# Kernel tuning notes

Hardware: AMD Instinct MI355X
Metric: run time of the kernel (lower is better)

Reference implementation:

```python
import jax, jax.numpy as jnp
import numpy as np

H = 128
OUT = 3
N_C = 50000
N_F = 150000
E_C = 400000
N_MP = 2


def _layernorm(x, g, b, eps=1e-5):
    mu = jnp.mean(x, axis=-1, keepdims=True)
    xc = x - mu
    var = jnp.mean(xc * xc, axis=-1, keepdims=True)
    return xc * jax.lax.rsqrt(var + eps) * g + b


def _seg_mean(v, idx, n):
    s = jax.ops.segment_sum(v, idx, num_segments=n)
    c = jax.ops.segment_sum(jnp.ones((v.shape[0],), v.dtype), idx, num_segments=n)
    return s / jnp.maximum(c, 1.0)[:, None]


def _mp_pass(x, ea, ei, n_nodes, eW0, eb0, eW1, eb1, eg, ebt, nW0, nb0, nW1, nb1, ng, nbt):
    src, dst = ei[0], ei[1]
    for i in range(N_MP):
        # edge update: gather endpoints, concat, 2-layer MLP, residual + LN
        t = jnp.concatenate([x[src], x[dst], ea], axis=1)  # [E, 3H]
        t = jax.nn.elu(t @ eW0[i] + eb0[i])
        t = t @ eW1[i] + eb1[i]
        ea = _layernorm(ea + t, eg[i], ebt[i])
        # scatter-mean aggregate edges to target nodes (EdgeAggregator)
        agg = _seg_mean(ea, dst, n_nodes)  # [N, H]
        xt = jnp.concatenate([x, agg], axis=1)  # [N, 2H]
        xt = jax.nn.elu(xt @ nW0[i] + nb0[i])
        xt = xt @ nW1[i] + nb1[i]
        x = _layernorm(x + xt, ng[i], nbt[i])
    return x, ea


def setup_inputs() -> dict:
    key = jax.random.key(0)
    ks = jax.random.split(key, 40)

    def nrm(k, shape, fan):
        return jax.random.normal(k, shape, jnp.float32) * np.float32(1.0 / np.sqrt(fan))

    inp = {}
    inp["x"] = jax.random.normal(ks[0], (N_C, H), jnp.float32)
    inp["edge_attr"] = jax.random.normal(ks[1], (E_C, H), jnp.float32)
    inp["pos_c"] = jax.random.uniform(ks[2], (N_C, 2), jnp.float32)
    inp["pos_f"] = jax.random.uniform(ks[3], (N_F, 2), jnp.float32)
    inp["edge_index_c"] = jax.random.randint(ks[4], (2, E_C), 0, N_C)
    clusters = jax.random.randint(ks[5], (N_F,), 0, N_C)
    inp["clusters"] = clusters
    # one f2c edge per fine node: row0 = fine idx, row1 = its coarse cluster
    inp["edge_index_f2c"] = jnp.stack([jnp.arange(N_F), clusters])
    # edge_up_mps params (stacked over N_MP layers)
    inp["eW0"] = nrm(ks[6], (N_MP, 3 * H, H), 3 * H)
    inp["eb0"] = jnp.zeros((N_MP, H), jnp.float32)
    inp["eW1"] = nrm(ks[7], (N_MP, H, H), H)
    inp["eb1"] = jnp.zeros((N_MP, H), jnp.float32)
    inp["eg"] = jnp.ones((N_MP, H), jnp.float32)
    inp["ebt"] = jnp.zeros((N_MP, H), jnp.float32)
    # node_up_mps params
    inp["nW0"] = nrm(ks[8], (N_MP, 2 * H, H), 2 * H)
    inp["nb0"] = jnp.zeros((N_MP, H), jnp.float32)
    inp["nW1"] = nrm(ks[9], (N_MP, H, H), H)
    inp["nb1"] = jnp.zeros((N_MP, H), jnp.float32)
    inp["ng"] = jnp.ones((N_MP, H), jnp.float32)
    inp["nbt"] = jnp.zeros((N_MP, H), jnp.float32)
    # edge_decoder_c2f_mlp
    inp["dW0"] = nrm(ks[10], (2, H), 2)
    inp["db0"] = jnp.zeros((H,), jnp.float32)
    inp["dW1"] = nrm(ks[11], (H, H), H)
    inp["db1"] = jnp.zeros((H,), jnp.float32)
    # upsample_mlp + norm
    inp["uW0"] = nrm(ks[12], (2 * H, H), 2 * H)
    inp["ub0"] = jnp.zeros((H,), jnp.float32)
    inp["uW1"] = nrm(ks[13], (H, H), H)
    inp["ub1"] = jnp.zeros((H,), jnp.float32)
    inp["ug"] = jnp.ones((H,), jnp.float32)
    inp["ubt"] = jnp.zeros((H,), jnp.float32)
    # output embedding
    inp["oW"] = nrm(ks[14], (H, OUT), H)
    inp["ob"] = jnp.zeros((OUT,), jnp.float32)
    return inp


def reference(x, edge_attr, pos_c, pos_f, edge_index_c, clusters, edge_index_f2c,
              eW0, eb0, eW1, eb1, eg, ebt, nW0, nb0, nW1, nb1, ng, nbt,
              dW0, db0, dW1, db1, uW0, ub0, uW1, ub1, ug, ubt, oW, ob):
    # coarse-level message passing (m = 0)
    x, ea = _mp_pass(x, edge_attr, edge_index_c, N_C,
                     eW0, eb0, eW1, eb1, eg, ebt, nW0, nb0, nW1, nb1, ng, nbt)
    # upsample coarse -> fine (depth = 2, l_char[0] = 1.0)
    c2f = edge_index_f2c[::-1]  # row0 = coarse idx, row1 = fine idx
    eac = (pos_c[c2f[0]] - pos_f[c2f[1]]) / 1.0  # [N_F, 2]
    eac = jax.nn.elu(eac @ dW0 + db0)
    eac = jax.nn.elu(eac @ dW1 + db1)
    xg = x[clusters]  # [N_F, H]
    t = jnp.concatenate([eac, xg], axis=1)
    t = jax.nn.elu(t @ uW0 + ub0)
    t = jax.nn.elu(t @ uW1 + ub1)
    t = _layernorm(eac + t, ug, ubt)
    x = _seg_mean(t, c2f[1], N_F)  # aggregate c2f edges onto fine nodes
    # fine-level message passing (m stays 0 in the original code -> same weights, same coarse edges)
    x, ea = _mp_pass(x, ea, edge_index_c, N_F,
                     eW0, eb0, eW1, eb1, eg, ebt, nW0, nb0, nW1, nb1, ng, nbt)
    x = jax.nn.elu(x @ oW + ob)
    return (x, edge_index_c)
```

## Files before the change

### kernel.cpp

```cpp
#include <hip/hip_runtime.h>


#define HD   128
#define NC   50000
#define NF   150000
#define ECNT 400000
#define OUTD 3
#define SCB  512
#define NB_SCAN ((NF + SCB - 1) / SCB)

typedef unsigned short u16;
typedef unsigned int   u32;
typedef short bf16x8 __attribute__((ext_vector_type(8)));
typedef float f32x4  __attribute__((ext_vector_type(4)));

__device__ __forceinline__ float bf2f(u32 u){ return __uint_as_float(u << 16); }
__device__ __forceinline__ u32 cvtpk(float a, float b){
  u32 r; asm("v_cvt_pk_bf16_f32 %0, %1, %2" : "=v"(r) : "v"(a), "v"(b)); return r;
}
__device__ __forceinline__ u16 f2bf(float f){ return (u16)cvtpk(f, f); }
__device__ __forceinline__ u32 addpk(u32 a, u32 b){
  return cvtpk(bf2f(a & 0xffffu) + bf2f(b & 0xffffu),
               __uint_as_float(a & 0xffff0000u) + __uint_as_float(b & 0xffff0000u));
}
__device__ __forceinline__ float eluf(float x){ return x > 0.f ? x : __expf(x) - 1.f; }
__device__ __forceinline__ int SW(int row, int byte){ return row * 256 + (byte ^ ((row & 7) << 4)); }


__global__ void prep_all_kernel(const float* __restrict__ eW0, const float* __restrict__ eW1,
                                const float* __restrict__ nW0, const float* __restrict__ nW1,
                                const float* __restrict__ uW0, const float* __restrict__ uW1,
                                const float* __restrict__ dW1,
                                u16* c_eW0, u16* c_eW1, u16* c_nW0, u16* c_nW1,
                                u16* c_uW0, u16* c_uW1, u16* c_dW1)
{
  int b = blockIdx.x;
  const float* src; u16* dst; int kb;
  if      (b <  384){ src = eW0; dst = c_eW0; kb = b * 2; }
  else if (b <  512){ src = eW1; dst = c_eW1; kb = (b - 384) * 2; }
  else if (b <  768){ src = nW0; dst = c_nW0; kb = (b - 512) * 2; }
  else if (b <  896){ src = nW1; dst = c_nW1; kb = (b - 768) * 2; }
  else if (b < 1024){ src = uW0; dst = c_uW0; kb = (b - 896) * 2; }
  else if (b < 1088){ src = uW1; dst = c_uW1; kb = (b - 1024) * 2; }
  else              { src = dW1; dst = c_dW1; kb = (b - 1088) * 2; }
  int t = threadIdx.x;
  int k = kb + (t >> 7), j = t & 127;
  dst[(((k >> 3) * HD + j) << 3) + (k & 7)] = f2bf(src[k * HD + j]);
}

__global__ void f32_to_bf16_vec(const float* __restrict__ in, u16* __restrict__ out, int n8){
  int i = blockIdx.x * blockDim.x + threadIdx.x;
  if (i >= n8) return;
  float4 f0 = ((const float4*)in)[i * 2];
  float4 f1 = ((const float4*)in)[i * 2 + 1];
  ((uint4*)out)[i] = make_uint4(cvtpk(f0.x,f0.y), cvtpk(f0.z,f0.w), cvtpk(f1.x,f1.y), cvtpk(f1.z,f1.w));
}

__global__ void deg_kernel(const int* __restrict__ ei, int* __restrict__ deg){
  int e = blockIdx.x * blockDim.x + threadIdx.x;
  if (e < ECNT) atomicAdd(&deg[ei[ECNT + e]], 1);
}

__global__ void scanA_kernel(const int* __restrict__ deg, int* __restrict__ part){
  __shared__ int s[SCB];
  int t = threadIdx.x, i = blockIdx.x * SCB + t;
  s[t] = (i < NF) ? deg[i] : 0;
  __syncthreads();
  for (int off = SCB/2; off; off >>= 1){ if (t < off) s[t] += s[t + off]; __syncthreads(); }
  if (t == 0) part[blockIdx.x] = s[0];
}

__global__ void scanB_kernel(int* __restrict__ part){
  __shared__ int s[SCB];
  int t = threadIdx.x;
  int v = (t < NB_SCAN) ? part[t] : 0;
  s[t] = v; __syncthreads();
  for (int off = 1; off < SCB; off <<= 1){
    int x = (t >= off) ? s[t - off] : 0;
    __syncthreads(); s[t] += x; __syncthreads();
  }
  if (t < NB_SCAN) part[t] = s[t] - v;
}

__global__ void scanC_kernel(const int* __restrict__ deg, const int* __restrict__ part,
                             int* __restrict__ rowptr){
  __shared__ int s[SCB];
  int t = threadIdx.x, i = blockIdx.x * SCB + t;
  int v = (i < NF) ? deg[i] : 0;
  s[t] = v; __syncthreads();
  for (int off = 1; off < SCB; off <<= 1){
    int x = (t >= off) ? s[t - off] : 0;
    __syncthreads(); s[t] += x; __syncthreads();
  }
  int excl = part[blockIdx.x] + s[t] - v;
  if (i < NF) rowptr[i] = excl;
  if (i == NF - 1) rowptr[NF] = excl + v;
}

__global__ void build_perm_kernel(const int* __restrict__ ei, int* __restrict__ cursor,
                                  int* __restrict__ perm, int* __restrict__ esrc,
                                  int* __restrict__ edst){
  int e = blockIdx.x * blockDim.x + threadIdx.x;
  if (e >= ECNT) return;
  int sI = ei[e], d = ei[ECNT + e];
  int p = atomicAdd(&cursor[d], 1);
  perm[p] = e; esrc[p] = sI; edst[p] = d;
}

__global__ void permute_ea_kernel(const float* __restrict__ ea_in, const int* __restrict__ perm,
                                  u16* __restrict__ ea_s){
  int i = blockIdx.x * blockDim.x + threadIdx.x;
  if (i >= ECNT * 16) return;
  int p = i >> 4, c = i & 15;
  int e = perm[p];
  const float4* src = (const float4*)(ea_in + (size_t)e * HD + c * 8);
  float4 f0 = src[0], f1 = src[1];
  ((uint4*)ea_s)[(size_t)p * 16 + c] =
      make_uint4(cvtpk(f0.x,f0.y), cvtpk(f0.z,f0.w), cvtpk(f1.x,f1.y), cvtpk(f1.z,f1.w));
}

template<int NOUT>
__global__ __launch_bounds__(256, 4)
void lin_kernel(const u16* __restrict__ Wa, const u16* __restrict__ Wb,
                const u16* __restrict__ x, u16* __restrict__ oA, u16* __restrict__ oB,
                int n_rows)
{
  __shared__ __align__(16) char ldsA[32 * 256];
  const int tid = threadIdx.x, lane = tid & 63, wid = tid >> 6;
  const int ln = lane & 15, kq = lane >> 4, ncol = wid * 32;

  const int row0 = blockIdx.x << 5;
  #pragma unroll
  for (int c = 0; c < 2; ++c){
    int i = tid + c * 256, row = i >> 4, kk = i & 15, rg = row0 + row;
    if (rg < n_rows)
      *(uint4*)(ldsA + SW(row, kk * 16)) = *(const uint4*)(x + (((size_t)rg) << 7) + (kk << 3));
  }
  __syncthreads();
  bf16x8 af[4][2];
  #pragma unroll
  for (int k0 = 0; k0 < 4; ++k0){
    af[k0][0] = *(const bf16x8*)(ldsA + SW(ln,      k0 * 64 + (kq << 4)));
    af[k0][1] = *(const bf16x8*)(ldsA + SW(16 + ln, k0 * 64 + (kq << 4)));
  }

  const u16* Ws[2] = {Wa, Wb};
  u16*       Os[2] = {oA, oB};
  const f32x4 zz = {0.f, 0.f, 0.f, 0.f};
  #pragma unroll
  for (int w = 0; w < NOUT; ++w){
    const u16* wp = Ws[w];
    asm volatile("" : "+v"(wp));
    uint4 bfr[4][2];
    #pragma unroll
    for (int k0 = 0; k0 < 4; ++k0)
      #pragma unroll
      for (int nt = 0; nt < 2; ++nt)
        bfr[k0][nt] = *(const uint4*)(wp + (((size_t)((k0*4 + kq)*HD + ncol + nt*16 + ln)) << 3));
    f32x4 cc[2][2] = {{zz, zz}, {zz, zz}};
    #pragma unroll
    for (int k0 = 0; k0 < 4; ++k0){
      bf16x8 w0 = __builtin_bit_cast(bf16x8, bfr[k0][0]);
      bf16x8 w1 = __builtin_bit_cast(bf16x8, bfr[k0][1]);
      cc[0][0] = __builtin_amdgcn_mfma_f32_16x16x32_bf16(af[k0][0], w0, cc[0][0], 0, 0, 0);
      cc[0][1] = __builtin_amdgcn_mfma_f32_16x16x32_bf16(af[k0][0], w1, cc[0][1], 0, 0, 0);
      cc[1][0] = __builtin_amdgcn_mfma_f32_16x16x32_bf16(af[k0][1], w0, cc[1][0], 0, 0, 0);
      cc[1][1] = __builtin_amdgcn_mfma_f32_16x16x32_bf16(af[k0][1], w1, cc[1][1], 0, 0, 0);
    }
    u16* op = Os[w];
    #pragma unroll
    for (int mi = 0; mi < 2; ++mi)
      #pragma unroll
      for (int nt = 0; nt < 2; ++nt)
        #pragma unroll
        for (int r = 0; r < 4; ++r){
          int rg = row0 + mi * 16 + kq * 4 + r;
          if (rg < n_rows) op[(size_t)rg * HD + ncol + nt * 16 + ln] = f2bf(cc[mi][nt][r]);
        }
  }
}

enum { M_EDGE = 0, M_NODE = 1, M_DEC12 = 2 };

template<int MODE>
__global__ __launch_bounds__(256, 4)
void mlp_kernel(const u16* __restrict__ W0c, const u16* __restrict__ W1c,
                const u16* __restrict__ W2c,
                const float* __restrict__ b0, const float* __restrict__ b1,
                const float* __restrict__ b2,
                const float* __restrict__ gw, const float* __restrict__ bw,
                const u16* __restrict__ tabA, const u16* __restrict__ addP,
                const u16* __restrict__ addQ, const u16* __restrict__ resid,
                const int* __restrict__ esrc, const int* __restrict__ edst,
                const int* __restrict__ rowptr, const u16* __restrict__ eatab,
                const int* __restrict__ clus,
                u16* __restrict__ outp, int n_rows,
                const float* __restrict__ dW0, const float* __restrict__ db0,
                const float* __restrict__ pos_c, const float* __restrict__ pos_f)
{
  constexpr bool RESLDS = (MODE == M_EDGE || MODE == M_DEC12);

  __shared__ __align__(16) char ldsA [32 * 256];
  __shared__ __align__(16) char ldsPQ[32 * 256];

  const int tid  = threadIdx.x;
  const int lane = tid & 63;
  const int wid  = tid >> 6;
  const int ln   = lane & 15, kq = lane >> 4;
  const int ncol = wid * 32;

  bf16x8 b1f[4][2];
  #pragma unroll
  for (int k0 = 0; k0 < 4; ++k0)
    #pragma unroll
    for (int nt = 0; nt < 2; ++nt)
      b1f[k0][nt] = *(const bf16x8*)(W0c + (((size_t)((k0*4 + kq)*HD + ncol + nt*16 + ln)) << 3));

  float b0v[2], b1v[2], b2v[2] = {0.f, 0.f};
  #pragma unroll
  for (int nt = 0; nt < 2; ++nt){ b0v[nt] = b0[ncol + nt*16 + ln]; b1v[nt] = b1[ncol + nt*16 + ln]; }
  if constexpr (MODE == M_DEC12){
    #pragma unroll
    for (int nt = 0; nt < 2; ++nt) b2v[nt] = b2[ncol + nt*16 + ln];
  }
  float gl0 = gw[lane], gl1 = gw[64 + lane], bt0 = bw[lane], bt1 = bw[64 + lane];

  const int row0 = blockIdx.x << 5;

  if constexpr (MODE == M_EDGE){
    #pragma unroll
    for (int c = 0; c < 2; ++c){
      int i = tid + c * 256, row = i >> 4, kk = i & 15, rg = row0 + row;
      *(uint4*)(ldsA + SW(row, kk * 16)) =
          *(const uint4*)(tabA + (((size_t)rg) << 7) + (kk << 3));
      int sI = esrc[rg], dI = edst[rg];
      uint4 p = *(const uint4*)(addP + (((size_t)sI) << 7) + (kk << 3));
      uint4 q = *(const uint4*)(addQ + (((size_t)dI) << 7) + (kk << 3));
      *(uint4*)(ldsPQ + SW(row, kk * 16)) =
          make_uint4(addpk(p.x,q.x), addpk(p.y,q.y), addpk(p.z,q.z), addpk(p.w,q.w));
    }
  } else if constexpr (MODE == M_NODE){
    #pragma unroll
    for (int c = 0; c < 2; ++c){
      int i = tid + c * 256, row = i >> 4, kk = i & 15, rg = row0 + row;
      if (rg < n_rows)
        *(uint4*)(ldsA + SW(row, kk * 16)) =
            *(const uint4*)(tabA + (((size_t)rg) << 7) + (kk << 3));
    }
  } else {
    #pragma unroll
    for (int c = 0; c < 2; ++c){
      int i = tid + c * 256, row = i >> 4, c8 = i & 15, rg = row0 + row;
      if (rg < n_rows){
        int cl = clus[rg];
        *(uint4*)(ldsPQ + SW(row, c8 * 16)) =
            *(const uint4*)(addP + (((size_t)cl) << 7) + (c8 << 3));
        float d0 = pos_c[cl * 2]     - pos_f[rg * 2];
        float d1 = pos_c[cl * 2 + 1] - pos_f[rg * 2 + 1];
        u32 wq[4];
        #pragma unroll
        for (int q = 0; q < 4; ++q){
          int cc = c8 * 8 + q * 2;
          float va = eluf(fmaf(d0, dW0[cc],     fmaf(d1, dW0[HD + cc],     db0[cc])));
          float vb = eluf(fmaf(d0, dW0[cc + 1], fmaf(d1, dW0[HD + cc + 1], db0[cc + 1])));
          wq[q] = cvtpk(va, vb);
        }
        *(uint4*)(ldsA + SW(row, c8 * 16)) = make_uint4(wq[0], wq[1], wq[2], wq[3]);
      }
    }
  }
  __syncthreads();

  const f32x4 zz = {0.f, 0.f, 0.f, 0.f};
  f32x4 c1[2][2] = {{zz, zz}, {zz, zz}};
  #pragma unroll
  for (int k0 = 0; k0 < 4; ++k0){
    bf16x8 a0 = *(const bf16x8*)(ldsA + SW(ln,      k0 * 64 + (kq << 4)));
    bf16x8 a1 = *(const bf16x8*)(ldsA + SW(16 + ln, k0 * 64 + (kq << 4)));
    c1[0][0] = __builtin_amdgcn_mfma_f32_16x16x32_bf16(a0, b1f[k0][0], c1[0][0], 0, 0, 0);
    c1[0][1] = __builtin_amdgcn_mfma_f32_16x16x32_bf16(a0, b1f[k0][1], c1[0][1], 0, 0, 0);
    c1[1][0] = __builtin_amdgcn_mfma_f32_16x16x32_bf16(a1, b1f[k0][0], c1[1][0], 0, 0, 0);
    c1[1][1] = __builtin_amdgcn_mfma_f32_16x16x32_bf16(a1, b1f[k0][1], c1[1][1], 0, 0, 0);
  }

  if constexpr (MODE == M_DEC12){
    __syncthreads();
    #pragma unroll
    for (int mi = 0; mi < 2; ++mi)
      #pragma unroll
      for (int nt = 0; nt < 2; ++nt)
        #pragma unroll
        for (int r = 0; r < 4; ++r){
          int row = mi * 16 + kq * 4 + r, col = ncol + nt * 16 + ln;
          *(u16*)(ldsA + SW(row, col * 2)) = f2bf(eluf(c1[mi][nt][r] + b0v[nt]));
        }
    __syncthreads();

    {
      const u16* w1p = W1c;
      asm volatile("" : "+v"(w1p));
      uint4 b2r[4][2];
      #pragma unroll
      for (int k0 = 0; k0 < 4; ++k0)
        #pragma unroll
        for (int nt = 0; nt < 2; ++nt)
          b2r[k0][nt] = *(const uint4*)(w1p + (((size_t)((k0*4 + kq)*HD + ncol + nt*16 + ln)) << 3));
      f32x4 c2[2][2] = {{zz, zz}, {zz, zz}};
      #pragma unroll
      for (int k0 = 0; k0 < 4; ++k0){
        bf16x8 a0 = *(const bf16x8*)(ldsA + SW(ln,      k0 * 64 + (kq << 4)));
        bf16x8 a1 = *(const bf16x8*)(ldsA + SW(16 + ln, k0 * 64 + (kq << 4)));
        bf16x8 w0 = __builtin_bit_cast(bf16x8, b2r[k0][0]);
        bf16x8 w1 = __builtin_bit_cast(bf16x8, b2r[k0][1]);
        c2[0][0] = __builtin_amdgcn_mfma_f32_16x16x32_bf16(a0, w0, c2[0][0], 0, 0, 0);
        c2[0][1] = __builtin_amdgcn_mfma_f32_16x16x32_bf16(a0, w1, c2[0][1], 0, 0, 0);
        c2[1][0] = __builtin_amdgcn_mfma_f32_16x16x32_bf16(a1, w0, c2[1][0], 0, 0, 0);
        c2[1][1] = __builtin_amdgcn_mfma_f32_16x16x32_bf16(a1, w1, c2[1][1], 0, 0, 0);
      }
      #pragma unroll
      for (int mi = 0; mi < 2; ++mi)
        #pragma unroll
        for (int nt = 0; nt < 2; ++nt)
          #pragma unroll
          for (int r = 0; r < 4; ++r){
            int row = mi * 16 + kq * 4 + r, col = ncol + nt * 16 + ln;
            u16* pp = (u16*)(ldsPQ + SW(row, col * 2));
            float pq = bf2f(*pp);
            *pp = f2bf(eluf(c2[mi][nt][r] + pq + b1v[nt]));
          }
    }
    __syncthreads();

    {
      const u16* w2p = W2c;
      asm volatile("" : "+v"(w2p));
      uint4 b3r[4][2];
      #pragma unroll
      for (int k0 = 0; k0 < 4; ++k0)
        #pragma unroll
        for (int nt = 0; nt < 2; ++nt)
          b3r[k0][nt] = *(const uint4*)(w2p + (((size_t)((k0*4 + kq)*HD + ncol + nt*16 + ln)) << 3));
      f32x4 c3[2][2] = {{zz, zz}, {zz, zz}};
      #pragma unroll
      for (int k0 = 0; k0 < 4; ++k0){
        bf16x8 a0 = *(const bf16x8*)(ldsPQ + SW(ln,      k0 * 64 + (kq << 4)));
        bf16x8 a1 = *(const bf16x8*)(ldsPQ + SW(16 + ln, k0 * 64 + (kq << 4)));
        bf16x8 w0 = __builtin_bit_cast(bf16x8, b3r[k0][0]);
        bf16x8 w1 = __builtin_bit_cast(bf16x8, b3r[k0][1]);
        c3[0][0] = __builtin_amdgcn_mfma_f32_16x16x32_bf16(a0, w0, c3[0][0], 0, 0, 0);
        c3[0][1] = __builtin_amdgcn_mfma_f32_16x16x32_bf16(a0, w1, c3[0][1], 0, 0, 0);
        c3[1][0] = __builtin_amdgcn_mfma_f32_16x16x32_bf16(a1, w0, c3[1][0], 0, 0, 0);
        c3[1][1] = __builtin_amdgcn_mfma_f32_16x16x32_bf16(a1, w1, c3[1][1], 0, 0, 0);
      }
      __syncthreads();
      #pragma unroll
      for (int mi = 0; mi < 2; ++mi)
        #pragma unroll
        for (int nt = 0; nt < 2; ++nt)
          #pragma unroll
          for (int r = 0; r < 4; ++r){
            int row = mi * 16 + kq * 4 + r, col = ncol + nt * 16 + ln;
            *(u16*)(ldsPQ + SW(row, col * 2)) = f2bf(eluf(c3[mi][nt][r] + b2v[nt]));
          }
    }
    __syncthreads();
  } else if constexpr (MODE == M_NODE){
    __syncthreads();
    const bool act = (row0 < NC);
    if (act){
      for (int s = 0; s < 8; ++s){
        int nd = wid * 8 + s, rg = row0 + nd;
        if (rg < n_rows){
          int rp0 = rowptr[rg], rp1 = rowptr[rg + 1];
          float s0 = 0.f, s1 = 0.f, t0 = 0.f, t1 = 0.f;
          int i2 = rp0;
          for (; i2 + 3 < rp1; i2 += 4){
            u32 ua = *(const u32*)(eatab + (((size_t) i2     ) << 7) + (lane << 1));
            u32 ub = *(const u32*)(eatab + (((size_t)(i2 + 1)) << 7) + (lane << 1));
            u32 uc = *(const u32*)(eatab + (((size_t)(i2 + 2)) << 7) + (lane << 1));
            u32 ud = *(const u32*)(eatab + (((size_t)(i2 + 3)) << 7) + (lane << 1));
            s0 += bf2f(ua & 0xffffu) + bf2f(ub & 0xffffu);
            s1 += bf2f(ua >> 16)     + bf2f(ub >> 16);
            t0 += bf2f(uc & 0xffffu) + bf2f(ud & 0xffffu);
            t1 += bf2f(uc >> 16)     + bf2f(ud >> 16);
          }
          for (; i2 < rp1; ++i2){
            u32 ua = *(const u32*)(eatab + (((size_t)i2) << 7) + (lane << 1));
            s0 += bf2f(ua & 0xffffu); s1 += bf2f(ua >> 16);
          }
          s0 += t0; s1 += t1;
          int dg = rp1 - rp0;
          float rd = 1.f / (float)(dg > 0 ? dg : 1);
          *(u32*)(ldsA + SW(nd, lane << 2)) = cvtpk(s0 * rd, s1 * rd);
        }
      }
    }
    __syncthreads();
    if (act){
      const u16* wbp = W1c;
      asm volatile("" : "+v"(wbp));
      uint4 bbr[4][2];
      #pragma unroll
      for (int k0 = 0; k0 < 4; ++k0)
        #pragma unroll
        for (int nt = 0; nt < 2; ++nt)
          bbr[k0][nt] = *(const uint4*)(wbp + (((size_t)((k0*4 + kq)*HD + ncol + nt*16 + ln)) << 3));
      #pragma unroll
      for (int k0 = 0; k0 < 4; ++k0){
        bf16x8 a0 = *(const bf16x8*)(ldsA + SW(ln,      k0 * 64 + (kq << 4)));
        bf16x8 a1 = *(const bf16x8*)(ldsA + SW(16 + ln, k0 * 64 + (kq << 4)));
        bf16x8 w0 = __builtin_bit_cast(bf16x8, bbr[k0][0]);
        bf16x8 w1 = __builtin_bit_cast(bf16x8, bbr[k0][1]);
        c1[0][0] = __builtin_amdgcn_mfma_f32_16x16x32_bf16(a0, w0, c1[0][0], 0, 0, 0);
        c1[0][1] = __builtin_amdgcn_mfma_f32_16x16x32_bf16(a0, w1, c1[0][1], 0, 0, 0);
        c1[1][0] = __builtin_amdgcn_mfma_f32_16x16x32_bf16(a1, w0, c1[1][0], 0, 0, 0);
        c1[1][1] = __builtin_amdgcn_mfma_f32_16x16x32_bf16(a1, w1, c1[1][1], 0, 0, 0);
      }
    }
    #pragma unroll
    for (int mi = 0; mi < 2; ++mi)
      #pragma unroll
      for (int nt = 0; nt < 2; ++nt)
        #pragma unroll
        for (int r = 0; r < 4; ++r){
          int row = mi * 16 + kq * 4 + r, col = ncol + nt * 16 + ln;
          *(u16*)(ldsPQ + SW(row, col * 2)) = f2bf(eluf(c1[mi][nt][r] + b0v[nt]));
        }
    __syncthreads();

    {
      const u16* w2p = W2c;
      asm volatile("" : "+v"(w2p));
      uint4 b3r[4][2];
      #pragma unroll
      for (int k0 = 0; k0 < 4; ++k0)
        #pragma unroll
        for (int nt = 0; nt < 2; ++nt)
          b3r[k0][nt] = *(const uint4*)(w2p + (((size_t)((k0*4 + kq)*HD + ncol + nt*16 + ln)) << 3));
      f32x4 c2[2][2] = {{zz, zz}, {zz, zz}};
      #pragma unroll
      for (int k0 = 0; k0 < 4; ++k0){
        bf16x8 a0 = *(const bf16x8*)(ldsPQ + SW(ln,      k0 * 64 + (kq << 4)));
        bf16x8 a1 = *(const bf16x8*)(ldsPQ + SW(16 + ln, k0 * 64 + (kq << 4)));
        bf16x8 w0 = __builtin_bit_cast(bf16x8, b3r[k0][0]);
        bf16x8 w1 = __builtin_bit_cast(bf16x8, b3r[k0][1]);
        c2[0][0] = __builtin_amdgcn_mfma_f32_16x16x32_bf16(a0, w0, c2[0][0], 0, 0, 0);
        c2[0][1] = __builtin_amdgcn_mfma_f32_16x16x32_bf16(a0, w1, c2[0][1], 0, 0, 0);
        c2[1][0] = __builtin_amdgcn_mfma_f32_16x16x32_bf16(a1, w0, c2[1][0], 0, 0, 0);
        c2[1][1] = __builtin_amdgcn_mfma_f32_16x16x32_bf16(a1, w1, c2[1][1], 0, 0, 0);
      }
      __syncthreads();
      #pragma unroll
      for (int mi = 0; mi < 2; ++mi)
        #pragma unroll
        for (int nt = 0; nt < 2; ++nt)
          #pragma unroll
          for (int r = 0; r < 4; ++r){
            int row = mi * 16 + kq * 4 + r, col = ncol + nt * 16 + ln;
            *(u16*)(ldsPQ + SW(row, col * 2)) = f2bf(c2[mi][nt][r] + b1v[nt]);
          }
    }
    __syncthreads();
  } else {
    const u16* w1p = W1c;
    asm volatile("" : "+v"(w1p));
    uint4 b2r[4][2];
    #pragma unroll
    for (int k0 = 0; k0 < 4; ++k0)
      #pragma unroll
      for (int nt = 0; nt < 2; ++nt)
        b2r[k0][nt] = *(const uint4*)(w1p + (((size_t)((k0*4 + kq)*HD + ncol + nt*16 + ln)) << 3));

    #pragma unroll
    for (int mi = 0; mi < 2; ++mi)
      #pragma unroll
      for (int nt = 0; nt < 2; ++nt)
        #pragma unroll
        for (int r = 0; r < 4; ++r){
          int row = mi * 16 + kq * 4 + r, col = ncol + nt * 16 + ln;
          u16* pp = (u16*)(ldsPQ + SW(row, col * 2));
          float pq = bf2f(*pp);
          *pp = f2bf(eluf(c1[mi][nt][r] + pq + b0v[nt]));
        }
    __syncthreads();

    f32x4 c2[2][2] = {{zz, zz}, {zz, zz}};
    #pragma unroll
    for (int k0 = 0; k0 < 4; ++k0){
      bf16x8 a0 = *(const bf16x8*)(ldsPQ + SW(ln,      k0 * 64 + (kq << 4)));
      bf16x8 a1 = *(const bf16x8*)(ldsPQ + SW(16 + ln, k0 * 64 + (kq << 4)));
      bf16x8 w0 = __builtin_bit_cast(bf16x8, b2r[k0][0]);
      bf16x8 w1 = __builtin_bit_cast(bf16x8, b2r[k0][1]);
      c2[0][0] = __builtin_amdgcn_mfma_f32_16x16x32_bf16(a0, w0, c2[0][0], 0, 0, 0);
      c2[0][1] = __builtin_amdgcn_mfma_f32_16x16x32_bf16(a0, w1, c2[0][1], 0, 0, 0);
      c2[1][0] = __builtin_amdgcn_mfma_f32_16x16x32_bf16(a1, w0, c2[1][0], 0, 0, 0);
      c2[1][1] = __builtin_amdgcn_mfma_f32_16x16x32_bf16(a1, w1, c2[1][1], 0, 0, 0);
    }
    __syncthreads();

    #pragma unroll
    for (int mi = 0; mi < 2; ++mi)
      #pragma unroll
      for (int nt = 0; nt < 2; ++nt)
        #pragma unroll
        for (int r = 0; r < 4; ++r){
          int row = mi * 16 + kq * 4 + r, col = ncol + nt * 16 + ln;
          *(u16*)(ldsPQ + SW(row, col * 2)) = f2bf(c2[mi][nt][r] + b1v[nt]);
        }
    __syncthreads();
  }

  #pragma unroll
  for (int rr = 0; rr < 8; ++rr){
    int e = wid * 8 + rr, rg = row0 + e;
    float v0 = bf2f(*(const u16*)(ldsPQ + SW(e, lane * 2)));
    float v1 = bf2f(*(const u16*)(ldsPQ + SW(e, (64 + lane) * 2)));
    if constexpr (RESLDS){
      v0 += bf2f(*(const u16*)(ldsA + SW(e, lane * 2)));
      v1 += bf2f(*(const u16*)(ldsA + SW(e, (64 + lane) * 2)));
    } else if (rg < n_rows){
      v0 += bf2f(resid[(((size_t)rg) << 7) + lane]);
      v1 += bf2f(resid[(((size_t)rg) << 7) + 64 + lane]);
    }
    float s = v0 + v1, q = v0 * v0 + v1 * v1;
    #pragma unroll
    for (int o = 32; o; o >>= 1){ s += __shfl_xor(s, o); q += __shfl_xor(q, o); }
    float mu  = s * (1.f / 128.f);
    float var = q * (1.f / 128.f) - mu * mu;
    float rs  = rsqrtf(var + 1e-5f);
    float y0 = (v0 - mu) * rs * gl0 + bt0;
    float y1 = (v1 - mu) * rs * gl1 + bt1;
    if (rg < n_rows){
      outp[(((size_t)rg) << 7) + lane]      = f2bf(y0);
      outp[(((size_t)rg) << 7) + 64 + lane] = f2bf(y1);
    }
  }
}

__global__ void outhead_kernel(const u16* __restrict__ x, const float* __restrict__ oW,
                               const float* __restrict__ ob, float* __restrict__ out){
  int row  = (blockIdx.x * blockDim.x + threadIdx.x) >> 6;
  int lane = threadIdx.x & 63;
  if (row >= NF) return;
  float x0 = bf2f(x[((size_t)row << 7) + lane]);
  float x1 = bf2f(x[((size_t)row << 7) + 64 + lane]);
  float s0 = x0 * oW[lane * 3 + 0] + x1 * oW[(64 + lane) * 3 + 0];
  float s1 = x0 * oW[lane * 3 + 1] + x1 * oW[(64 + lane) * 3 + 1];
  float s2 = x0 * oW[lane * 3 + 2] + x1 * oW[(64 + lane) * 3 + 2];
  #pragma unroll
  for (int o = 32; o; o >>= 1){
    s0 += __shfl_xor(s0, o); s1 += __shfl_xor(s1, o); s2 += __shfl_xor(s2, o);
  }
  if (lane == 0){
    out[row * 3 + 0] = eluf(s0 + ob[0]);
    out[row * 3 + 1] = eluf(s1 + ob[1]);
    out[row * 3 + 2] = eluf(s2 + ob[2]);
  }
}

__global__ void idxcopy_kernel(const int* __restrict__ ei, float* __restrict__ out){
  int i = blockIdx.x * blockDim.x + threadIdx.x;
  if (i < 2 * ECNT) out[i] = (float)ei[i];
}

extern "C" void kernel_launch(void* const* d_in, const int* in_sizes, int n_in,
                              void* d_out, int out_size, void* d_ws, size_t ws_size,
                              hipStream_t stream)
{
  const float* x_in  = (const float*)d_in[0];
  const float* ea_in = (const float*)d_in[1];
  const float* pos_c = (const float*)d_in[2];
  const float* pos_f = (const float*)d_in[3];
  const int*   ei    = (const int*)d_in[4];
  const int*   clus  = (const int*)d_in[5];
  const float* eW0 = (const float*)d_in[7];
  const float* eb0 = (const float*)d_in[8];
  const float* eW1 = (const float*)d_in[9];
  const float* eb1 = (const float*)d_in[10];
  const float* eg  = (const float*)d_in[11];
  const float* ebt = (const float*)d_in[12];
  const float* nW0 = (const float*)d_in[13];
  const float* nb0 = (const float*)d_in[14];
  const float* nW1 = (const float*)d_in[15];
  const float* nb1 = (const float*)d_in[16];
  const float* ng  = (const float*)d_in[17];
  const float* nbt = (const float*)d_in[18];
  const float* dW0 = (const float*)d_in[19];
  const float* db0 = (const float*)d_in[20];
  const float* dW1 = (const float*)d_in[21];
  const float* db1 = (const float*)d_in[22];
  const float* uW0 = (const float*)d_in[23];
  const float* ub0 = (const float*)d_in[24];
  const float* uW1 = (const float*)d_in[25];
  const float* ub1 = (const float*)d_in[26];
  const float* ug  = (const float*)d_in[27];
  const float* ubt = (const float*)d_in[28];
  const float* oW  = (const float*)d_in[29];
  const float* ob  = (const float*)d_in[30];

  char* w = (char*)d_ws;
  auto alloc = [&](size_t bytes) -> char* {
    char* p = w; w += (bytes + 255) & ~(size_t)255; return p;
  };
  u16*   ea_s   = (u16*)alloc((size_t)ECNT * HD * 2);
  u16*   xa     = (u16*)alloc((size_t)NC * HD * 2);
  u16*   xb     = (u16*)alloc((size_t)NF * HD * 2);
  u16*   P      = (u16*)alloc((size_t)NC * HD * 2);
  u16*   Q      = (u16*)alloc((size_t)NC * HD * 2);
  u16*   XU     = (u16*)alloc((size_t)NC * HD * 2);
  int*   deg    = (int*)alloc((size_t)NF * 4);
  int*   rowptr = (int*)alloc((size_t)(NF + 1) * 4);
  int*   cursor = (int*)alloc((size_t)NF * 4);
  int*   perm   = (int*)alloc((size_t)ECNT * 4);
  int*   esrc   = (int*)alloc((size_t)ECNT * 4);
  int*   edst   = (int*)alloc((size_t)ECNT * 4);
  int*   part   = (int*)alloc((size_t)SCB * 4);
  u16*   c_eW0  = (u16*)alloc((size_t)2 * 384 * HD * 2);
  u16*   c_eW1  = (u16*)alloc((size_t)2 * HD * HD * 2);
  u16*   c_nW0  = (u16*)alloc((size_t)2 * 256 * HD * 2);
  u16*   c_nW1  = (u16*)alloc((size_t)2 * HD * HD * 2);
  u16*   c_uW0  = (u16*)alloc((size_t)256 * HD * 2);
  u16*   c_uW1  = (u16*)alloc((size_t)HD * HD * 2);
  u16*   c_dW1  = (u16*)alloc((size_t)HD * HD * 2);

  prep_all_kernel<<<1152, 256, 0, stream>>>(eW0, eW1, nW0, nW1, uW0, uW1, dW1,
                                            c_eW0, c_eW1, c_nW0, c_nW1, c_uW0, c_uW1, c_dW1);
  f32_to_bf16_vec<<<(NC * HD / 8 + 255) / 256, 256, 0, stream>>>(x_in, xa, NC * HD / 8);

  hipMemsetAsync(deg, 0, (size_t)NF * 4, stream);
  deg_kernel<<<(ECNT + 255) / 256, 256, 0, stream>>>(ei, deg);
  scanA_kernel<<<NB_SCAN, SCB, 0, stream>>>(deg, part);
  scanB_kernel<<<1, SCB, 0, stream>>>(part);
  scanC_kernel<<<NB_SCAN, SCB, 0, stream>>>(deg, part, rowptr);
  hipMemcpyAsync(cursor, rowptr, (size_t)NF * 4, hipMemcpyDeviceToDevice, stream);
  build_perm_kernel<<<(ECNT + 255) / 256, 256, 0, stream>>>(ei, cursor, perm, esrc, edst);
  permute_ea_kernel<<<(ECNT * 16 + 255) / 256, 256, 0, stream>>>(ea_in, perm, ea_s);

  auto grd = [](int rows){ return (rows + 31) / 32; };
  const int KS = 16 * HD * 8;

  auto mp_iter = [&](u16* x, int n, int i){
    int npq = n < NC ? n : NC;
    lin_kernel<2><<<grd(npq), 256, 0, stream>>>(
      c_eW0 + (size_t)i*384*HD, c_eW0 + (size_t)i*384*HD + KS, x, P, Q, npq);
    mlp_kernel<M_EDGE><<<grd(ECNT), 256, 0, stream>>>(
      c_eW0 + (size_t)i*384*HD + 2*KS, c_eW1 + (size_t)i*HD*HD, nullptr,
      eb0 + i*HD, eb1 + i*HD, nullptr, eg + i*HD, ebt + i*HD,
      ea_s, P, Q, nullptr, esrc, edst, nullptr, nullptr, nullptr,
      ea_s, ECNT, nullptr, nullptr, nullptr, nullptr);
    mlp_kernel<M_NODE><<<grd(n), 256, 0, stream>>>(
      c_nW0 + (size_t)i*256*HD, c_nW0 + (size_t)i*256*HD + KS, c_nW1 + (size_t)i*HD*HD,
      nb0 + i*HD, nb1 + i*HD, nullptr, ng + i*HD, nbt + i*HD,
      x, nullptr, nullptr, x, nullptr, nullptr, rowptr, ea_s, nullptr,
      x, n, nullptr, nullptr, nullptr, nullptr);
  };

  mp_iter(xa, NC, 0);
  mp_iter(xa, NC, 1);

  lin_kernel<1><<<grd(NC), 256, 0, stream>>>(
    c_uW0 + KS, nullptr, xa, XU, nullptr, NC);
  mlp_kernel<M_DEC12><<<grd(NF), 256, 0, stream>>>(
    c_dW1, c_uW0, c_uW1,
    db1, ub0, ub1, ug, ubt,
    nullptr, XU, nullptr, nullptr,
    nullptr, nullptr, nullptr, nullptr, clus,
    xb, NF, dW0, db0, pos_c, pos_f);

  mp_iter(xb, NF, 0);
  mp_iter(xb, NF, 1);

  float* out = (float*)d_out;
  outhead_kernel<<<(NF + 3) / 4, 256, 0, stream>>>(xb, oW, ob, out);
  idxcopy_kernel<<<(2 * ECNT + 255) / 256, 256, 0, stream>>>(ei, out + (size_t)NF * OUTD);
}
```

Before: 888.3 us.

## Fuse next-layer projections into node/decoder epilogues and compute LayerNorm from MFMA registers

The following layer's per-node linear projections (P/Q for the edge MLP, XU for upsampling) are now computed inside the node and decoder MLP kernels from the freshly normalized rows held in LDS. This removes the separate lin_kernel launches and their re-read of x. The mlp kernel also computes LayerNorm statistics straight from the accumulator fragments through a small LDS reduction, instead of a separate row-wise pass, and the ea permutation uses one wavefront per row. The costs are more registers and LDS per block plus extra synchronisation, which may lower occupancy.

```diff
diff --git a/kernel.cpp b/kernel.cpp
--- a/kernel.cpp
+++ b/kernel.cpp
@@ -109,21 +109,18 @@
 
 __global__ void permute_ea_kernel(const float* __restrict__ ea_in, const int* __restrict__ perm,
                                   u16* __restrict__ ea_s){
-  int i = blockIdx.x * blockDim.x + threadIdx.x;
-  if (i >= ECNT * 16) return;
-  int p = i >> 4, c = i & 15;
+  int p = (blockIdx.x << 2) + (threadIdx.x >> 6);
+  int lane = threadIdx.x & 63;
+  if (p >= ECNT) return;
   int e = perm[p];
-  const float4* src = (const float4*)(ea_in + (size_t)e * HD + c * 8);
-  float4 f0 = src[0], f1 = src[1];
-  ((uint4*)ea_s)[(size_t)p * 16 + c] =
-      make_uint4(cvtpk(f0.x,f0.y), cvtpk(f0.z,f0.w), cvtpk(f1.x,f1.y), cvtpk(f1.z,f1.w));
-}
-
-template<int NOUT>
+  float2 f = *(const float2*)(ea_in + (((size_t)e) << 7) + (lane << 1));
+  *(u32*)(ea_s + (((size_t)p) << 7) + (lane << 1)) = cvtpk(f.x, f.y);
+}
+
 __global__ __launch_bounds__(256, 4)
-void lin_kernel(const u16* __restrict__ Wa, const u16* __restrict__ Wb,
-                const u16* __restrict__ x, u16* __restrict__ oA, u16* __restrict__ oB,
-                int n_rows)
+void lin2_kernel(const u16* __restrict__ Wa, const u16* __restrict__ Wb,
+                 const u16* __restrict__ x, u16* __restrict__ oA, u16* __restrict__ oB,
+                 int n_rows)
 {
   __shared__ __align__(16) char ldsA[32 * 256];
   const int tid = threadIdx.x, lane = tid & 63, wid = tid >> 6;
@@ -143,12 +140,11 @@
     af[k0][0] = *(const bf16x8*)(ldsA + SW(ln,      k0 * 64 + (kq << 4)));
     af[k0][1] = *(const bf16x8*)(ldsA + SW(16 + ln, k0 * 64 + (kq << 4)));
   }
-
   const u16* Ws[2] = {Wa, Wb};
   u16*       Os[2] = {oA, oB};
   const f32x4 zz = {0.f, 0.f, 0.f, 0.f};
   #pragma unroll
-  for (int w = 0; w < NOUT; ++w){
+  for (int w = 0; w < 2; ++w){
     const u16* wp = Ws[w];
     asm volatile("" : "+v"(wp));
     uint4 bfr[4][2];
@@ -182,7 +178,7 @@
 
 enum { M_EDGE = 0, M_NODE = 1, M_DEC12 = 2 };
 
-template<int MODE>
+template<int MODE, int FUSE>
 __global__ __launch_bounds__(256, 4)
 void mlp_kernel(const u16* __restrict__ W0c, const u16* __restrict__ W1c,
                 const u16* __restrict__ W2c,
@@ -190,18 +186,22 @@
                 const float* __restrict__ b2,
                 const float* __restrict__ gw, const float* __restrict__ bw,
                 const u16* __restrict__ tabA, const u16* __restrict__ addP,
-                const u16* __restrict__ addQ, const u16* __restrict__ resid,
+                const u16* __restrict__ addQ,
                 const int* __restrict__ esrc, const int* __restrict__ edst,
                 const int* __restrict__ rowptr, const u16* __restrict__ eatab,
                 const int* __restrict__ clus,
                 u16* __restrict__ outp, int n_rows,
                 const float* __restrict__ dW0, const float* __restrict__ db0,
-                const float* __restrict__ pos_c, const float* __restrict__ pos_f)
+                const float* __restrict__ pos_c, const float* __restrict__ pos_f,
+                const u16* __restrict__ Wf0, const u16* __restrict__ Wf1,
+                u16* __restrict__ oF0, u16* __restrict__ oF1, int fuse_n)
 {
-  constexpr bool RESLDS = (MODE == M_EDGE || MODE == M_DEC12);
-
-  __shared__ __align__(16) char ldsA [32 * 256];
-  __shared__ __align__(16) char ldsPQ[32 * 256];
+  constexpr bool ELU2 = (MODE == M_DEC12);
+
+  __shared__ __align__(16) char  ldsA [32 * 256];
+  __shared__ __align__(16) char  ldsPQ[32 * 256];
+  __shared__ float ldsSQ[32 * 8];
+  __shared__ float ldsM [32 * 2];
 
   const int tid  = threadIdx.x;
   const int lane = tid & 63;
@@ -216,16 +216,18 @@
     for (int nt = 0; nt < 2; ++nt)
       b1f[k0][nt] = *(const bf16x8*)(W0c + (((size_t)((k0*4 + kq)*HD + ncol + nt*16 + ln)) << 3));
 
-  float b0v[2], b1v[2], b2v[2] = {0.f, 0.f};
-  #pragma unroll
-  for (int nt = 0; nt < 2; ++nt){ b0v[nt] = b0[ncol + nt*16 + ln]; b1v[nt] = b1[ncol + nt*16 + ln]; }
-  if constexpr (MODE == M_DEC12){
-    #pragma unroll
-    for (int nt = 0; nt < 2; ++nt) b2v[nt] = b2[ncol + nt*16 + ln];
-  }
-  float gl0 = gw[lane], gl1 = gw[64 + lane], bt0 = bw[lane], bt1 = bw[64 + lane];
+  float b0v[2], b1v[2], bfin[2], gv[2], btv[2];
+  #pragma unroll
+  for (int nt = 0; nt < 2; ++nt){
+    int col = ncol + nt*16 + ln;
+    b0v[nt] = b0[col]; b1v[nt] = b1[col];
+    bfin[nt] = (MODE == M_DEC12) ? b2[col] : b1v[nt];
+    gv[nt] = gw[col]; btv[nt] = bw[col];
+  }
 
   const int row0 = blockIdx.x << 5;
+  const f32x4 zz = {0.f, 0.f, 0.f, 0.f};
+  f32x4 cf[2][2];
 
   if constexpr (MODE == M_EDGE){
     #pragma unroll
@@ -239,6 +241,50 @@
       *(uint4*)(ldsPQ + SW(row, kk * 16)) =
           make_uint4(addpk(p.x,q.x), addpk(p.y,q.y), addpk(p.z,q.z), addpk(p.w,q.w));
     }
+    __syncthreads();
+    cf[0][0]=zz; cf[0][1]=zz; cf[1][0]=zz; cf[1][1]=zz;
+    #pragma unroll
+    for (int k0 = 0; k0 < 4; ++k0){
+      bf16x8 a0 = *(const bf16x8*)(ldsA + SW(ln,      k0 * 64 + (kq << 4)));
+      bf16x8 a1 = *(const bf16x8*)(ldsA + SW(16 + ln, k0 * 64 + (kq << 4)));
+      cf[0][0] = __builtin_amdgcn_mfma_f32_16x16x32_bf16(a0, b1f[k0][0], cf[0][0], 0, 0, 0);
+      cf[0][1] = __builtin_amdgcn_mfma_f32_16x16x32_bf16(a0, b1f[k0][1], cf[0][1], 0, 0, 0);
+      cf[1][0] = __builtin_amdgcn_mfma_f32_16x16x32_bf16(a1, b1f[k0][0], cf[1][0], 0, 0, 0);
+      cf[1][1] = __builtin_amdgcn_mfma_f32_16x16x32_bf16(a1, b1f[k0][1], cf[1][1], 0, 0, 0);
+    }
+    #pragma unroll
+    for (int mi = 0; mi < 2; ++mi)
+      #pragma unroll
+      for (int nt = 0; nt < 2; ++nt)
+        #pragma unroll
+        for (int r = 0; r < 4; ++r){
+          int row = mi * 16 + kq * 4 + r, col = ncol + nt * 16 + ln;
+          u16* pp = (u16*)(ldsPQ + SW(row, col * 2));
+          *pp = f2bf(eluf(cf[mi][nt][r] + bf2f(*pp) + b0v[nt]));
+        }
+    __syncthreads();
+    {
+      const u16* w1p = W1c;
+      asm volatile("" : "+v"(w1p));
+      uint4 b2r[4][2];
+      #pragma unroll
+      for (int k0 = 0; k0 < 4; ++k0)
+        #pragma unroll
+        for (int nt = 0; nt < 2; ++nt)
+          b2r[k0][nt] = *(const uint4*)(w1p + (((size_t)((k0*4 + kq)*HD + ncol + nt*16 + ln)) << 3));
+      cf[0][0]=zz; cf[0][1]=zz; cf[1][0]=zz; cf[1][1]=zz;
+      #pragma unroll
+      for (int k0 = 0; k0 < 4; ++k0){
+        bf16x8 a0 = *(const bf16x8*)(ldsPQ + SW(ln,      k0 * 64 + (kq << 4)));
+        bf16x8 a1 = *(const bf16x8*)(ldsPQ + SW(16 + ln, k0 * 64 + (kq << 4)));
+        bf16x8 w0 = __builtin_bit_cast(bf16x8, b2r[k0][0]);
+        bf16x8 w1 = __builtin_bit_cast(bf16x8, b2r[k0][1]);
+        cf[0][0] = __builtin_amdgcn_mfma_f32_16x16x32_bf16(a0, w0, cf[0][0], 0, 0, 0);
+        cf[0][1] = __builtin_amdgcn_mfma_f32_16x16x32_bf16(a0, w1, cf[0][1], 0, 0, 0);
+        cf[1][0] = __builtin_amdgcn_mfma_f32_16x16x32_bf16(a1, w0, cf[1][0], 0, 0, 0);
+        cf[1][1] = __builtin_amdgcn_mfma_f32_16x16x32_bf16(a1, w1, cf[1][1], 0, 0, 0);
+      }
+    }
   } else if constexpr (MODE == M_NODE){
     #pragma unroll
     for (int c = 0; c < 2; ++c){
@@ -247,125 +293,6 @@
         *(uint4*)(ldsA + SW(row, kk * 16)) =
             *(const uint4*)(tabA + (((size_t)rg) << 7) + (kk << 3));
     }
-  } else {
-    #pragma unroll
-    for (int c = 0; c < 2; ++c){
-      int i = tid + c * 256, row = i >> 4, c8 = i & 15, rg = row0 + row;
-      if (rg < n_rows){
-        int cl = clus[rg];
-        *(uint4*)(ldsPQ + SW(row, c8 * 16)) =
-            *(const uint4*)(addP + (((size_t)cl) << 7) + (c8 << 3));
-        float d0 = pos_c[cl * 2]     - pos_f[rg * 2];
-        float d1 = pos_c[cl * 2 + 1] - pos_f[rg * 2 + 1];
-        u32 wq[4];
-        #pragma unroll
-        for (int q = 0; q < 4; ++q){
-          int cc = c8 * 8 + q * 2;
-          float va = eluf(fmaf(d0, dW0[cc],     fmaf(d1, dW0[HD + cc],     db0[cc])));
-          float vb = eluf(fmaf(d0, dW0[cc + 1], fmaf(d1, dW0[HD + cc + 1], db0[cc + 1])));
-          wq[q] = cvtpk(va, vb);
-        }
-        *(uint4*)(ldsA + SW(row, c8 * 16)) = make_uint4(wq[0], wq[1], wq[2], wq[3]);
-      }
-    }
-  }
-  __syncthreads();
-
-  const f32x4 zz = {0.f, 0.f, 0.f, 0.f};
-  f32x4 c1[2][2] = {{zz, zz}, {zz, zz}};
-  #pragma unroll
-  for (int k0 = 0; k0 < 4; ++k0){
-    bf16x8 a0 = *(const bf16x8*)(ldsA + SW(ln,      k0 * 64 + (kq << 4)));
-    bf16x8 a1 = *(const bf16x8*)(ldsA + SW(16 + ln, k0 * 64 + (kq << 4)));
-    c1[0][0] = __builtin_amdgcn_mfma_f32_16x16x32_bf16(a0, b1f[k0][0], c1[0][0], 0, 0, 0);
-    c1[0][1] = __builtin_amdgcn_mfma_f32_16x16x32_bf16(a0, b1f[k0][1], c1[0][1], 0, 0, 0);
-    c1[1][0] = __builtin_amdgcn_mfma_f32_16x16x32_bf16(a1, b1f[k0][0], c1[1][0], 0, 0, 0);
-    c1[1][1] = __builtin_amdgcn_mfma_f32_16x16x32_bf16(a1, b1f[k0][1], c1[1][1], 0, 0, 0);
-  }
-
-  if constexpr (MODE == M_DEC12){
-    __syncthreads();
-    #pragma unroll
-    for (int mi = 0; mi < 2; ++mi)
-      #pragma unroll
-      for (int nt = 0; nt < 2; ++nt)
-        #pragma unroll
-        for (int r = 0; r < 4; ++r){
-          int row = mi * 16 + kq * 4 + r, col = ncol + nt * 16 + ln;
-          *(u16*)(ldsA + SW(row, col * 2)) = f2bf(eluf(c1[mi][nt][r] + b0v[nt]));
-        }
-    __syncthreads();
-
-    {
-      const u16* w1p = W1c;
-      asm volatile("" : "+v"(w1p));
-      uint4 b2r[4][2];
-      #pragma unroll
-      for (int k0 = 0; k0 < 4; ++k0)
-        #pragma unroll
-        for (int nt = 0; nt < 2; ++nt)
-          b2r[k0][nt] = *(const uint4*)(w1p + (((size_t)((k0*4 + kq)*HD + ncol + nt*16 + ln)) << 3));
-      f32x4 c2[2][2] = {{zz, zz}, {zz, zz}};
-      #pragma unroll
-      for (int k0 = 0; k0 < 4; ++k0){
-        bf16x8 a0 = *(const bf16x8*)(ldsA + SW(ln,      k0 * 64 + (kq << 4)));
-        bf16x8 a1 = *(const bf16x8*)(ldsA + SW(16 + ln, k0 * 64 + (kq << 4)));
-        bf16x8 w0 = __builtin_bit_cast(bf16x8, b2r[k0][0]);
-        bf16x8 w1 = __builtin_bit_cast(bf16x8, b2r[k0][1]);
-        c2[0][0] = __builtin_amdgcn_mfma_f32_16x16x32_bf16(a0, w0, c2[0][0], 0, 0, 0);
-        c2[0][1] = __builtin_amdgcn_mfma_f32_16x16x32_bf16(a0, w1, c2[0][1], 0, 0, 0);
-        c2[1][0] = __builtin_amdgcn_mfma_f32_16x16x32_bf16(a1, w0, c2[1][0], 0, 0, 0);
-        c2[1][1] = __builtin_amdgcn_mfma_f32_16x16x32_bf16(a1, w1, c2[1][1], 0, 0, 0);
-      }
-      #pragma unroll
-      for (int mi = 0; mi < 2; ++mi)
-        #pragma unroll
-        for (int nt = 0; nt < 2; ++nt)
-          #pragma unroll
-          for (int r = 0; r < 4; ++r){
-            int row = mi * 16 + kq * 4 + r, col = ncol + nt * 16 + ln;
-            u16* pp = (u16*)(ldsPQ + SW(row, col * 2));
-            float pq = bf2f(*pp);
-            *pp = f2bf(eluf(c2[mi][nt][r] + pq + b1v[nt]));
-          }
-    }
-    __syncthreads();
-
-    {
-      const u16* w2p = W2c;
-      asm volatile("" : "+v"(w2p));
-      uint4 b3r[4][2];
-      #pragma unroll
-      for (int k0 = 0; k0 < 4; ++k0)
-        #pragma unroll
-        for (int nt = 0; nt < 2; ++nt)
-          b3r[k0][nt] = *(const uint4*)(w2p + (((size_t)((k0*4 + kq)*HD + ncol + nt*16 + ln)) << 3));
-      f32x4 c3[2][2] = {{zz, zz}, {zz, zz}};
-      #pragma unroll
-      for (int k0 = 0; k0 < 4; ++k0){
-        bf16x8 a0 = *(const bf16x8*)(ldsPQ + SW(ln,      k0 * 64 + (kq << 4)));
-        bf16x8 a1 = *(const bf16x8*)(ldsPQ + SW(16 + ln, k0 * 64 + (kq << 4)));
-        bf16x8 w0 = __builtin_bit_cast(bf16x8, b3r[k0][0]);
-        bf16x8 w1 = __builtin_bit_cast(bf16x8, b3r[k0][1]);
-        c3[0][0] = __builtin_amdgcn_mfma_f32_16x16x32_bf16(a0, w0, c3[0][0], 0, 0, 0);
-        c3[0][1] = __builtin_amdgcn_mfma_f32_16x16x32_bf16(a0, w1, c3[0][1], 0, 0, 0);
-        c3[1][0] = __builtin_amdgcn_mfma_f32_16x16x32_bf16(a1, w0, c3[1][0], 0, 0, 0);
-        c3[1][1] = __builtin_amdgcn_mfma_f32_16x16x32_bf16(a1, w1, c3[1][1], 0, 0, 0);
-      }
-      __syncthreads();
-      #pragma unroll
-      for (int mi = 0; mi < 2; ++mi)
-        #pragma unroll
-        for (int nt = 0; nt < 2; ++nt)
-          #pragma unroll
-          for (int r = 0; r < 4; ++r){
-            int row = mi * 16 + kq * 4 + r, col = ncol + nt * 16 + ln;
-            *(u16*)(ldsPQ + SW(row, col * 2)) = f2bf(eluf(c3[mi][nt][r] + b2v[nt]));
-          }
-    }
-    __syncthreads();
-  } else if constexpr (MODE == M_NODE){
-    __syncthreads();
     const bool act = (row0 < NC);
     if (act){
       for (int s = 0; s < 8; ++s){
@@ -391,11 +318,21 @@
           s0 += t0; s1 += t1;
           int dg = rp1 - rp0;
           float rd = 1.f / (float)(dg > 0 ? dg : 1);
-          *(u32*)(ldsA + SW(nd, lane << 2)) = cvtpk(s0 * rd, s1 * rd);
+          *(u32*)(ldsPQ + SW(nd, lane << 2)) = cvtpk(s0 * rd, s1 * rd);
         }
       }
     }
     __syncthreads();
+    cf[0][0]=zz; cf[0][1]=zz; cf[1][0]=zz; cf[1][1]=zz;
+    #pragma unroll
+    for (int k0 = 0; k0 < 4; ++k0){
+      bf16x8 a0 = *(const bf16x8*)(ldsA + SW(ln,      k0 * 64 + (kq << 4)));
+      bf16x8 a1 = *(const bf16x8*)(ldsA + SW(16 + ln, k0 * 64 + (kq << 4)));
+      cf[0][0] = __builtin_amdgcn_mfma_f32_16x16x32_bf16(a0, b1f[k0][0], cf[0][0], 0, 0, 0);
+      cf[0][1] = __builtin_amdgcn_mfma_f32_16x16x32_bf16(a0, b1f[k0][1], cf[0][1], 0, 0, 0);
+      cf[1][0] = __builtin_amdgcn_mfma_f32_16x16x32_bf16(a1, b1f[k0][0], cf[1][0], 0, 0, 0);
+      cf[1][1] = __builtin_amdgcn_mfma_f32_16x16x32_bf16(a1, b1f[k0][1], cf[1][1], 0, 0, 0);
+    }
     if (act){
       const u16* wbp = W1c;
       asm volatile("" : "+v"(wbp));
@@ -407,16 +344,17 @@
           bbr[k0][nt] = *(const uint4*)(wbp + (((size_t)((k0*4 + kq)*HD + ncol + nt*16 + ln)) << 3));
       #pragma unroll
       for (int k0 = 0; k0 < 4; ++k0){
-        bf16x8 a0 = *(const bf16x8*)(ldsA + SW(ln,      k0 * 64 + (kq << 4)));
-        bf16x8 a1 = *(const bf16x8*)(ldsA + SW(16 + ln, k0 * 64 + (kq << 4)));
+        bf16x8 a0 = *(const bf16x8*)(ldsPQ + SW(ln,      k0 * 64 + (kq << 4)));
+        bf16x8 a1 = *(const bf16x8*)(ldsPQ + SW(16 + ln, k0 * 64 + (kq << 4)));
         bf16x8 w0 = __builtin_bit_cast(bf16x8, bbr[k0][0]);
         bf16x8 w1 = __builtin_bit_cast(bf16x8, bbr[k0][1]);
-        c1[0][0] = __builtin_amdgcn_mfma_f32_16x16x32_bf16(a0, w0, c1[0][0], 0, 0, 0);
-        c1[0][1] = __builtin_amdgcn_mfma_f32_16x16x32_bf16(a0, w1, c1[0][1], 0, 0, 0);
-        c1[1][0] = __builtin_amdgcn_mfma_f32_16x16x32_bf16(a1, w0, c1[1][0], 0, 0, 0);
-        c1[1][1] = __builtin_amdgcn_mfma_f32_16x16x32_bf16(a1, w1, c1[1][1], 0, 0, 0);
-      }
-    }
+        cf[0][0] = __builtin_amdgcn_mfma_f32_16x16x32_bf16(a0, w0, cf[0][0], 0, 0, 0);
+        cf[0][1] = __builtin_amdgcn_mfma_f32_16x16x32_bf16(a0, w1, cf[0][1], 0, 0, 0);
+        cf[1][0] = __builtin_amdgcn_mfma_f32_16x16x32_bf16(a1, w0, cf[1][0], 0, 0, 0);
+        cf[1][1] = __builtin_amdgcn_mfma_f32_16x16x32_bf16(a1, w1, cf[1][1], 0, 0, 0);
+      }
+    }
+    __syncthreads();
     #pragma unroll
     for (int mi = 0; mi < 2; ++mi)
       #pragma unroll
@@ -424,10 +362,9 @@
         #pragma unroll
         for (int r = 0; r < 4; ++r){
           int row = mi * 16 + kq * 4 + r, col = ncol + nt * 16 + ln;
-          *(u16*)(ldsPQ + SW(row, col * 2)) = f2bf(eluf(c1[mi][nt][r] + b0v[nt]));
+          *(u16*)(ldsPQ + SW(row, col * 2)) = f2bf(eluf(cf[mi][nt][r] + b0v[nt]));
         }
     __syncthreads();
-
     {
       const u16* w2p = W2c;
       asm volatile("" : "+v"(w2p));
@@ -437,19 +374,83 @@
         #pragma unroll
         for (int nt = 0; nt < 2; ++nt)
           b3r[k0][nt] = *(const uint4*)(w2p + (((size_t)((k0*4 + kq)*HD + ncol + nt*16 + ln)) << 3));
-      f32x4 c2[2][2] = {{zz, zz}, {zz, zz}};
+      cf[0][0]=zz; cf[0][1]=zz; cf[1][0]=zz; cf[1][1]=zz;
       #pragma unroll
       for (int k0 = 0; k0 < 4; ++k0){
         bf16x8 a0 = *(const bf16x8*)(ldsPQ + SW(ln,      k0 * 64 + (kq << 4)));
         bf16x8 a1 = *(const bf16x8*)(ldsPQ + SW(16 + ln, k0 * 64 + (kq << 4)));
         bf16x8 w0 = __builtin_bit_cast(bf16x8, b3r[k0][0]);
         bf16x8 w1 = __builtin_bit_cast(bf16x8, b3r[k0][1]);
-        c2[0][0] = __builtin_amdgcn_mfma_f32_16x16x32_bf16(a0, w0, c2[0][0], 0, 0, 0);
-        c2[0][1] = __builtin_amdgcn_mfma_f32_16x16x32_bf16(a0, w1, c2[0][1], 0, 0, 0);
-        c2[1][0] = __builtin_amdgcn_mfma_f32_16x16x32_bf16(a1, w0, c2[1][0], 0, 0, 0);
-        c2[1][1] = __builtin_amdgcn_mfma_f32_16x16x32_bf16(a1, w1, c2[1][1], 0, 0, 0);
-      }
-      __syncthreads();
+        cf[0][0] = __builtin_amdgcn_mfma_f32_16x16x32_bf16(a0, w0, cf[0][0], 0, 0, 0);
+        cf[0][1] = __builtin_amdgcn_mfma_f32_16x16x32_bf16(a0, w1, cf[0][1], 0, 0, 0);
+        cf[1][0] = __builtin_amdgcn_mfma_f32_16x16x32_bf16(a1, w0, cf[1][0], 0, 0, 0);
+        cf[1][1] = __builtin_amdgcn_mfma_f32_16x16x32_bf16(a1, w1, cf[1][1], 0, 0, 0);
+      }
+    }
+  } else {
+    #pragma unroll
+    for (int c = 0; c < 2; ++c){
+      int i = tid + c * 256, row = i >> 4, c8 = i & 15, rg = row0 + row;
+      if (rg < n_rows){
+        int cl = clus[rg];
+        *(uint4*)(ldsPQ + SW(row, c8 * 16)) =
+            *(const uint4*)(addP + (((size_t)cl) << 7) + (c8 << 3));
+        float d0 = pos_c[cl * 2]     - pos_f[rg * 2];
+        float d1 = pos_c[cl * 2 + 1] - pos_f[rg * 2 + 1];
+        u32 wq[4];
+        #pragma unroll
+        for (int q = 0; q < 4; ++q){
+          int cc = c8 * 8 + q * 2;
+          float va = eluf(fmaf(d0, dW0[cc],     fmaf(d1, dW0[HD + cc],     db0[cc])));
+          float vb = eluf(fmaf(d0, dW0[cc + 1], fmaf(d1, dW0[HD + cc + 1], db0[cc + 1])));
+          wq[q] = cvtpk(va, vb);
+        }
+        *(uint4*)(ldsA + SW(row, c8 * 16)) = make_uint4(wq[0], wq[1], wq[2], wq[3]);
+      }
+    }
+    __syncthreads();
+    cf[0][0]=zz; cf[0][1]=zz; cf[1][0]=zz; cf[1][1]=zz;
+    #pragma unroll
+    for (int k0 = 0; k0 < 4; ++k0){
+      bf16x8 a0 = *(const bf16x8*)(ldsA + SW(ln,      k0 * 64 + (kq << 4)));
+      bf16x8 a1 = *(const bf16x8*)(ldsA + SW(16 + ln, k0 * 64 + (kq << 4)));
+      cf[0][0] = __builtin_amdgcn_mfma_f32_16x16x32_bf16(a0, b1f[k0][0], cf[0][0], 0, 0, 0);
+      cf[0][1] = __builtin_amdgcn_mfma_f32_16x16x32_bf16(a0, b1f[k0][1], cf[0][1], 0, 0, 0);
+      cf[1][0] = __builtin_amdgcn_mfma_f32_16x16x32_bf16(a1, b1f[k0][0], cf[1][0], 0, 0, 0);
+      cf[1][1] = __builtin_amdgcn_mfma_f32_16x16x32_bf16(a1, b1f[k0][1], cf[1][1], 0, 0, 0);
+    }
+    __syncthreads();
+    #pragma unroll
+    for (int mi = 0; mi < 2; ++mi)
+      #pragma unroll
+      for (int nt = 0; nt < 2; ++nt)
+        #pragma unroll
+        for (int r = 0; r < 4; ++r){
+          int row = mi * 16 + kq * 4 + r, col = ncol + nt * 16 + ln;
+          *(u16*)(ldsA + SW(row, col * 2)) = f2bf(eluf(cf[mi][nt][r] + b0v[nt]));
+        }
+    __syncthreads();
+    {
+      const u16* w1p = W1c;
+      asm volatile("" : "+v"(w1p));
+      uint4 b2r[4][2];
+      #pragma unroll
+      for (int k0 = 0; k0 < 4; ++k0)
+        #pragma unroll
+        for (int nt = 0; nt < 2; ++nt)
+          b2r[k0][nt] = *(const uint4*)(w1p + (((size_t)((k0*4 + kq)*HD + ncol + nt*16 + ln)) << 3));
+      cf[0][0]=zz; cf[0][1]=zz; cf[1][0]=zz; cf[1][1]=zz;
+      #pragma unroll
+      for (int k0 = 0; k0 < 4; ++k0){
+        bf16x8 a0 = *(const bf16x8*)(ldsA + SW(ln,      k0 * 64 + (kq << 4)));
+        bf16x8 a1 = *(const bf16x8*)(ldsA + SW(16 + ln, k0 * 64 + (kq << 4)));
+        bf16x8 w0 = __builtin_bit_cast(bf16x8, b2r[k0][0]);
+        bf16x8 w1 = __builtin_bit_cast(bf16x8, b2r[k0][1]);
+        cf[0][0] = __builtin_amdgcn_mfma_f32_16x16x32_bf16(a0, w0, cf[0][0], 0, 0, 0);
+        cf[0][1] = __builtin_amdgcn_mfma_f32_16x16x32_bf16(a0, w1, cf[0][1], 0, 0, 0);
+        cf[1][0] = __builtin_amdgcn_mfma_f32_16x16x32_bf16(a1, w0, cf[1][0], 0, 0, 0);
+        cf[1][1] = __builtin_amdgcn_mfma_f32_16x16x32_bf16(a1, w1, cf[1][1], 0, 0, 0);
+      }
       #pragma unroll
       for (int mi = 0; mi < 2; ++mi)
         #pragma unroll
@@ -457,82 +458,144 @@
           #pragma unroll
           for (int r = 0; r < 4; ++r){
             int row = mi * 16 + kq * 4 + r, col = ncol + nt * 16 + ln;
-            *(u16*)(ldsPQ + SW(row, col * 2)) = f2bf(c2[mi][nt][r] + b1v[nt]);
+            u16* pp = (u16*)(ldsPQ + SW(row, col * 2));
+            *pp = f2bf(eluf(cf[mi][nt][r] + bf2f(*pp) + b1v[nt]));
           }
     }
     __syncthreads();
-  } else {
-    const u16* w1p = W1c;
-    asm volatile("" : "+v"(w1p));
-    uint4 b2r[4][2];
-    #pragma unroll
-    for (int k0 = 0; k0 < 4; ++k0)
-      #pragma unroll
-      for (int nt = 0; nt < 2; ++nt)
-        b2r[k0][nt] = *(const uint4*)(w1p + (((size_t)((k0*4 + kq)*HD + ncol + nt*16 + ln)) << 3));
-
+    {
+      const u16* w2p = W2c;
+      asm volatile("" : "+v"(w2p));
+      uint4 b3r[4][2];
+      #pragma unroll
+      for (int k0 = 0; k0 < 4; ++k0)
+        #pragma unroll
+        for (int nt = 0; nt < 2; ++nt)
+          b3r[k0][nt] = *(const uint4*)(w2p + (((size_t)((k0*4 + kq)*HD + ncol + nt*16 + ln)) << 3));
+      cf[0][0]=zz; cf[0][1]=zz; cf[1][0]=zz; cf[1][1]=zz;
+      #pragma unroll
+      for (int k0 = 0; k0 < 4; ++k0){
+        bf16x8 a0 = *(const bf16x8*)(ldsPQ + SW(ln,      k0 * 64 + (kq << 4)));
+        bf16x8 a1 = *(const bf16x8*)(ldsPQ + SW(16 + ln, k0 * 64 + (kq << 4)));
+        bf16x8 w0 = __builtin_bit_cast(bf16x8, b3r[k0][0]);
+        bf16x8 w1 = __builtin_bit_cast(bf16x8, b3r[k0][1]);
+        cf[0][0] = __builtin_amdgcn_mfma_f32_16x16x32_bf16(a0, w0, cf[0][0], 0, 0, 0);
+        cf[0][1] = __builtin_amdgcn_mfma_f32_16x16x32_bf16(a0, w1, cf[0][1], 0, 0, 0);
+        cf[1][0] = __builtin_amdgcn_mfma_f32_16x16x32_bf16(a1, w0, cf[1][0], 0, 0, 0);
+        cf[1][1] = __builtin_amdgcn_mfma_f32_16x16x32_bf16(a1, w1, cf[1][1], 0, 0, 0);
+      }
+    }
+  }
+
+  #pragma unroll
+  for (int mi = 0; mi < 2; ++mi)
+    #pragma unroll
+    for (int nt = 0; nt < 2; ++nt)
+      #pragma unroll
+      for (int r = 0; r < 4; ++r){
+        int row = mi * 16 + kq * 4 + r, col = ncol + nt * 16 + ln;
+        float v = cf[mi][nt][r] + bfin[nt];
+        if constexpr (ELU2) v = eluf(v);
+        v += bf2f(*(const u16*)(ldsA + SW(row, col * 2)));
+        cf[mi][nt][r] = v;
+      }
+  float sp[8], qp[8];
+  #pragma unroll
+  for (int mi = 0; mi < 2; ++mi)
+    #pragma unroll
+    for (int r = 0; r < 4; ++r){
+      int ri = mi * 4 + r;
+      float a = cf[mi][0][r], b = cf[mi][1][r];
+      sp[ri] = a + b; qp[ri] = a * a + b * b;
+    }
+  #pragma unroll
+  for (int off = 1; off < 16; off <<= 1)
+    #pragma unroll
+    for (int ri = 0; ri < 8; ++ri){
+      sp[ri] += __shfl_xor(sp[ri], off);
+      qp[ri] += __shfl_xor(qp[ri], off);
+    }
+  if (ln == 0){
     #pragma unroll
     for (int mi = 0; mi < 2; ++mi)
       #pragma unroll
-      for (int nt = 0; nt < 2; ++nt)
-        #pragma unroll
-        for (int r = 0; r < 4; ++r){
-          int row = mi * 16 + kq * 4 + r, col = ncol + nt * 16 + ln;
-          u16* pp = (u16*)(ldsPQ + SW(row, col * 2));
-          float pq = bf2f(*pp);
-          *pp = f2bf(eluf(c1[mi][nt][r] + pq + b0v[nt]));
-        }
-    __syncthreads();
-
-    f32x4 c2[2][2] = {{zz, zz}, {zz, zz}};
-    #pragma unroll
-    for (int k0 = 0; k0 < 4; ++k0){
-      bf16x8 a0 = *(const bf16x8*)(ldsPQ + SW(ln,      k0 * 64 + (kq << 4)));
-      bf16x8 a1 = *(const bf16x8*)(ldsPQ + SW(16 + ln, k0 * 64 + (kq << 4)));
-      bf16x8 w0 = __builtin_bit_cast(bf16x8, b2r[k0][0]);
-      bf16x8 w1 = __builtin_bit_cast(bf16x8, b2r[k0][1]);
-      c2[0][0] = __builtin_amdgcn_mfma_f32_16x16x32_bf16(a0, w0, c2[0][0], 0, 0, 0);
-      c2[0][1] = __builtin_amdgcn_mfma_f32_16x16x32_bf16(a0, w1, c2[0][1], 0, 0, 0);
-      c2[1][0] = __builtin_amdgcn_mfma_f32_16x16x32_bf16(a1, w0, c2[1][0], 0, 0, 0);
-      c2[1][1] = __builtin_amdgcn_mfma_f32_16x16x32_bf16(a1, w1, c2[1][1], 0, 0, 0);
-    }
-    __syncthreads();
-
-    #pragma unroll
-    for (int mi = 0; mi < 2; ++mi)
-      #pragma unroll
-      for (int nt = 0; nt < 2; ++nt)
-        #pragma unroll
-        for (int r = 0; r < 4; ++r){
-          int row = mi * 16 + kq * 4 + r, col = ncol + nt * 16 + ln;
-          *(u16*)(ldsPQ + SW(row, col * 2)) = f2bf(c2[mi][nt][r] + b1v[nt]);
-        }
-    __syncthreads();
-  }
-
-  #pragma unroll
-  for (int rr = 0; rr < 8; ++rr){
-    int e = wid * 8 + rr, rg = row0 + e;
-    float v0 = bf2f(*(const u16*)(ldsPQ + SW(e, lane * 2)));
-    float v1 = bf2f(*(const u16*)(ldsPQ + SW(e, (64 + lane) * 2)));
-    if constexpr (RESLDS){
-      v0 += bf2f(*(const u16*)(ldsA + SW(e, lane * 2)));
-      v1 += bf2f(*(const u16*)(ldsA + SW(e, (64 + lane) * 2)));
-    } else if (rg < n_rows){
-      v0 += bf2f(resid[(((size_t)rg) << 7) + lane]);
-      v1 += bf2f(resid[(((size_t)rg) << 7) + 64 + lane]);
-    }
-    float s = v0 + v1, q = v0 * v0 + v1 * v1;
-    #pragma unroll
-    for (int o = 32; o; o >>= 1){ s += __shfl_xor(s, o); q += __shfl_xor(q, o); }
+      for (int r = 0; r < 4; ++r){
+        int row = mi * 16 + kq * 4 + r;
+        ldsSQ[row * 8 + wid * 2]     = sp[mi * 4 + r];
+        ldsSQ[row * 8 + wid * 2 + 1] = qp[mi * 4 + r];
+      }
+  }
+  __syncthreads();
+  if (tid < 32){
+    float s = ldsSQ[tid*8+0] + ldsSQ[tid*8+2] + ldsSQ[tid*8+4] + ldsSQ[tid*8+6];
+    float q = ldsSQ[tid*8+1] + ldsSQ[tid*8+3] + ldsSQ[tid*8+5] + ldsSQ[tid*8+7];
     float mu  = s * (1.f / 128.f);
     float var = q * (1.f / 128.f) - mu * mu;
-    float rs  = rsqrtf(var + 1e-5f);
-    float y0 = (v0 - mu) * rs * gl0 + bt0;
-    float y1 = (v1 - mu) * rs * gl1 + bt1;
-    if (rg < n_rows){
-      outp[(((size_t)rg) << 7) + lane]      = f2bf(y0);
-      outp[(((size_t)rg) << 7) + 64 + lane] = f2bf(y1);
+    ldsM[tid * 2]     = mu;
+    ldsM[tid * 2 + 1] = rsqrtf(var + 1e-5f);
+  }
+  __syncthreads();
+  #pragma unroll
+  for (int mi = 0; mi < 2; ++mi)
+    #pragma unroll
+    for (int r = 0; r < 4; ++r){
+      int row = mi * 16 + kq * 4 + r, rg = row0 + row;
+      float mu = ldsM[row * 2], rs = ldsM[row * 2 + 1];
+      #pragma unroll
+      for (int nt = 0; nt < 2; ++nt){
+        int col = ncol + nt * 16 + ln;
+        float y = (cf[mi][nt][r] - mu) * rs * gv[nt] + btv[nt];
+        u16 yb = f2bf(y);
+        if (MODE == M_EDGE || rg < n_rows)
+          outp[(((size_t)rg) << 7) + col] = yb;
+        if constexpr (FUSE > 0)
+          *(u16*)(ldsA + SW(row, col * 2)) = yb;
+      }
+    }
+
+  if constexpr (FUSE > 0){
+    __syncthreads();
+    if (row0 < fuse_n){
+      bf16x8 af[4][2];
+      #pragma unroll
+      for (int k0 = 0; k0 < 4; ++k0){
+        af[k0][0] = *(const bf16x8*)(ldsA + SW(ln,      k0 * 64 + (kq << 4)));
+        af[k0][1] = *(const bf16x8*)(ldsA + SW(16 + ln, k0 * 64 + (kq << 4)));
+      }
+      const u16* Ws[2] = {Wf0, Wf1};
+      u16*       Os[2] = {oF0, oF1};
+      #pragma unroll
+      for (int w = 0; w < FUSE; ++w){
+        const u16* wp = Ws[w];
+        asm volatile("" : "+v"(wp));
+        uint4 bfr[4][2];
+        #pragma unroll
+        for (int k0 = 0; k0 < 4; ++k0)
+          #pragma unroll
+          for (int nt = 0; nt < 2; ++nt)
+            bfr[k0][nt] = *(const uint4*)(wp + (((size_t)((k0*4 + kq)*HD + ncol + nt*16 + ln)) << 3));
+        f32x4 cc[2][2] = {{zz, zz}, {zz, zz}};
+        #pragma unroll
+        for (int k0 = 0; k0 < 4; ++k0){
+          bf16x8 w0 = __builtin_bit_cast(bf16x8, bfr[k0][0]);
+          bf16x8 w1 = __builtin_bit_cast(bf16x8, bfr[k0][1]);
+          cc[0][0] = __builtin_amdgcn_mfma_f32_16x16x32_bf16(af[k0][0], w0, cc[0][0], 0, 0, 0);
+          cc[0][1] = __builtin_amdgcn_mfma_f32_16x16x32_bf16(af[k0][0], w1, cc[0][1], 0, 0, 0);
+          cc[1][0] = __builtin_amdgcn_mfma_f32_16x16x32_bf16(af[k0][1], w0, cc[1][0], 0, 0, 0);
+          cc[1][1] = __builtin_amdgcn_mfma_f32_16x16x32_bf16(af[k0][1], w1, cc[1][1], 0, 0, 0);
+        }
+        u16* op = Os[w];
+        #pragma unroll
+        for (int mi = 0; mi < 2; ++mi)
+          #pragma unroll
+          for (int nt = 0; nt < 2; ++nt)
+            #pragma unroll
+            for (int r = 0; r < 4; ++r){
+              int rg = row0 + mi * 16 + kq * 4 + r;
+              if (rg < fuse_n)
+                op[(size_t)rg * HD + ncol + nt * 16 + ln] = f2bf(cc[mi][nt][r]);
+            }
+      }
     }
   }
 }
@@ -634,41 +697,60 @@
   scanC_kernel<<<NB_SCAN, SCB, 0, stream>>>(deg, part, rowptr);
   hipMemcpyAsync(cursor, rowptr, (size_t)NF * 4, hipMemcpyDeviceToDevice, stream);
   build_perm_kernel<<<(ECNT + 255) / 256, 256, 0, stream>>>(ei, cursor, perm, esrc, edst);
-  permute_ea_kernel<<<(ECNT * 16 + 255) / 256, 256, 0, stream>>>(ea_in, perm, ea_s);
+  permute_ea_kernel<<<(ECNT + 3) / 4, 256, 0, stream>>>(ea_in, perm, ea_s);
 
   auto grd = [](int rows){ return (rows + 31) / 32; };
   const int KS = 16 * HD * 8;
 
-  auto mp_iter = [&](u16* x, int n, int i){
-    int npq = n < NC ? n : NC;
-    lin_kernel<2><<<grd(npq), 256, 0, stream>>>(
-      c_eW0 + (size_t)i*384*HD, c_eW0 + (size_t)i*384*HD + KS, x, P, Q, npq);
-    mlp_kernel<M_EDGE><<<grd(ECNT), 256, 0, stream>>>(
-      c_eW0 + (size_t)i*384*HD + 2*KS, c_eW1 + (size_t)i*HD*HD, nullptr,
+  auto eslice = [&](int i, int s){ return c_eW0 + (size_t)i * 384 * HD + (size_t)s * KS; };
+
+  auto edge = [&](u16* x_unused, int i){
+    mlp_kernel<M_EDGE, 0><<<grd(ECNT), 256, 0, stream>>>(
+      eslice(i, 2), c_eW1 + (size_t)i*HD*HD, nullptr,
       eb0 + i*HD, eb1 + i*HD, nullptr, eg + i*HD, ebt + i*HD,
-      ea_s, P, Q, nullptr, esrc, edst, nullptr, nullptr, nullptr,
-      ea_s, ECNT, nullptr, nullptr, nullptr, nullptr);
-    mlp_kernel<M_NODE><<<grd(n), 256, 0, stream>>>(
-      c_nW0 + (size_t)i*256*HD, c_nW0 + (size_t)i*256*HD + KS, c_nW1 + (size_t)i*HD*HD,
-      nb0 + i*HD, nb1 + i*HD, nullptr, ng + i*HD, nbt + i*HD,
-      x, nullptr, nullptr, x, nullptr, nullptr, rowptr, ea_s, nullptr,
-      x, n, nullptr, nullptr, nullptr, nullptr);
+      ea_s, P, Q, esrc, edst, nullptr, nullptr, nullptr,
+      ea_s, ECNT, nullptr, nullptr, nullptr, nullptr,
+      nullptr, nullptr, nullptr, nullptr, 0);
   };
-
-  mp_iter(xa, NC, 0);
-  mp_iter(xa, NC, 1);
-
-  lin_kernel<1><<<grd(NC), 256, 0, stream>>>(
-    c_uW0 + KS, nullptr, xa, XU, nullptr, NC);
-  mlp_kernel<M_DEC12><<<grd(NF), 256, 0, stream>>>(
+  auto node = [&](u16* x, int n, int i, int F,
+                  const u16* Wf0, const u16* Wf1, u16* oF0, u16* oF1){
+    if (F == 2)
+      mlp_kernel<M_NODE, 2><<<grd(n), 256, 0, stream>>>(
+        c_nW0 + (size_t)i*256*HD, c_nW0 + (size_t)i*256*HD + KS, c_nW1 + (size_t)i*HD*HD,
+        nb0 + i*HD, nb1 + i*HD, nullptr, ng + i*HD, nbt + i*HD,
+        x, nullptr, nullptr, nullptr, nullptr, rowptr, ea_s, nullptr,
+        x, n, nullptr, nullptr, nullptr, nullptr, Wf0, Wf1, oF0, oF1, NC);
+    else if (F == 1)
+      mlp_kernel<M_NODE, 1><<<grd(n), 256, 0, stream>>>(
+        c_nW0 + (size_t)i*256*HD, c_nW0 + (size_t)i*256*HD + KS, c_nW1 + (size_t)i*HD*HD,
+        nb0 + i*HD, nb1 + i*HD, nullptr, ng + i*HD, nbt + i*HD,
+        x, nullptr, nullptr, nullptr, nullptr, rowptr, ea_s, nullptr,
+        x, n, nullptr, nullptr, nullptr, nullptr, Wf0, nullptr, oF0, nullptr, NC);
+    else
+      mlp_kernel<M_NODE, 0><<<grd(n), 256, 0, stream>>>(
+        c_nW0 + (size_t)i*256*HD, c_nW0 + (size_t)i*256*HD + KS, c_nW1 + (size_t)i*HD*HD,
+        nb0 + i*HD, nb1 + i*HD, nullptr, ng + i*HD, nbt + i*HD,
+        x, nullptr, nullptr, nullptr, nullptr, rowptr, ea_s, nullptr,
+        x, n, nullptr, nullptr, nullptr, nullptr, nullptr, nullptr, nullptr, nullptr, 0);
+  };
+
+  lin2_kernel<<<grd(NC), 256, 0, stream>>>(eslice(0,0), eslice(0,1), xa, P, Q, NC);
+  edge(xa, 0);
+  node(xa, NC, 0, 2, eslice(1,0), eslice(1,1), P, Q);
+  edge(xa, 1);
+  node(xa, NC, 1, 1, c_uW0 + KS, nullptr, XU, nullptr);
+
+  mlp_kernel<M_DEC12, 2><<<grd(NF), 256, 0, stream>>>(
     c_dW1, c_uW0, c_uW1,
     db1, ub0, ub1, ug, ubt,
-    nullptr, XU, nullptr, nullptr,
-    nullptr, nullptr, nullptr, nullptr, clus,
-    xb, NF, dW0, db0, pos_c, pos_f);
-
-  mp_iter(xb, NF, 0);
-  mp_iter(xb, NF, 1);
+    nullptr, XU, nullptr, nullptr, nullptr, nullptr, nullptr, clus,
+    xb, NF, dW0, db0, pos_c, pos_f,
+    eslice(0,0), eslice(0,1), P, Q, NC);
+
+  edge(xb, 0);
+  node(xb, NF, 0, 2, eslice(1,0), eslice(1,1), P, Q);
+  edge(xb, 1);
+  node(xb, NF, 1, 0, nullptr, nullptr, nullptr, nullptr);
 
   float* out = (float*)d_out;
   outhead_kernel<<<(NF + 3) / 4, 256, 0, stream>>>(xb, oW, ob, out);
```

Result: faster. 850.9 us (-4.2%).
